# Performance work log

Measured on AMD Instinct MI355X. Metric: run time of the kernel, lower is better.

The kernel has to match this reference:

```python
import jax, jax.numpy as jnp
import numpy as np

B = 64       # graphs per batch
NPG = 1000   # nodes per graph
EPG = 8000   # edges per graph
F = 128      # num_node_features


def _lin_w(k, fi, fo):
    s = 1.0 / np.sqrt(fi)
    return jax.random.uniform(k, (fi, fo), jnp.float32, -s, s)


def setup_inputs() -> dict:
    key = jax.random.key(0)
    ks = jax.random.split(key, 40)
    N, E = B * NPG, B * EPG

    def edges(k1, k2):
        src = jax.random.randint(k1, (E,), 0, NPG)
        dst = jax.random.randint(k2, (E,), 0, NPG)
        off = (jnp.arange(E) // EPG) * NPG  # keep edges within each graph
        return jnp.stack([src + off, dst + off]).astype(jnp.int32)

    inp = {
        'x0': jax.random.normal(ks[0], (N, F), jnp.float32),
        'edge_attr0': jax.random.uniform(ks[1], (E, 4), jnp.float32),
        'edge_index0': edges(ks[2], ks[3]),
        'x1': jax.random.normal(ks[4], (N, F), jnp.float32),
        'edge_attr1': jax.random.uniform(ks[5], (E, 4), jnp.float32),
        'edge_index1': edges(ks[6], ks[7]),
        'batch0': (jnp.arange(N) // NPG).astype(jnp.int32),
        'batch1': (jnp.arange(N) // NPG).astype(jnp.int32),
        'num_graphs': B,
    }
    # GCNConv weights/biases (6 convs, all F->F)
    names = ['1A', '1B', '1C', '1D', '2', '3']
    for i, nm in enumerate(names):
        inp['W' + nm] = _lin_w(ks[8 + i], F, F)
        inp['b' + nm] = jnp.zeros((F,), jnp.float32)
    # SAGPooling score GNN (GraphConv: lin_rel with bias, lin_root no bias), 3F -> 1
    inp['Ws_rel'] = _lin_w(ks[20], 3 * F, 1)
    inp['bs_rel'] = jnp.zeros((1,), jnp.float32)
    inp['Ws_root'] = _lin_w(ks[21], 3 * F, 1)
    # MLP: 6F -> 32 -> 8 -> 2
    inp['Wm1'] = _lin_w(ks[22], 6 * F, 32)
    inp['bm1'] = jnp.zeros((32,), jnp.float32)
    inp['Wm2'] = _lin_w(ks[23], 32, 8)
    inp['bm2'] = jnp.zeros((8,), jnp.float32)
    inp['Wm3'] = _lin_w(ks[24], 8, 2)
    inp['bm3'] = jnp.zeros((2,), jnp.float32)
    return inp


def gcn_conv(x, W, b, row, col, ew):
    # PyG GCNConv: add self-loops (w=1), symmetric norm, gather->scatter-add
    N = x.shape[0]
    h = x @ W  # [N, F]
    sl = jnp.arange(N)
    row_f = jnp.concatenate([row, sl])
    col_f = jnp.concatenate([col, sl])
    w_f = jnp.concatenate([ew, jnp.ones((N,), x.dtype)])
    deg = jax.ops.segment_sum(w_f, col_f, num_segments=N)
    dinv = jnp.where(deg > 0, jax.lax.rsqrt(jnp.maximum(deg, 1e-12)), 0.0)
    norm = (dinv[row_f] * w_f * dinv[col_f])[:, None]
    return jax.ops.segment_sum(h[row_f] * norm, col_f, num_segments=N) + b


def reference(x0, edge_attr0, edge_index0, x1, edge_attr1, edge_index1,
              batch0, batch1, num_graphs,
              W1A, b1A, W1B, b1B, W1C, b1C, W1D, b1D, W2, b2, W3, b3,
              Ws_rel, bs_rel, Ws_root, Wm1, bm1, Wm2, bm2, Wm3, bm3):
    Bn = int(num_graphs)

    def branch(x, ea, ei):
        row, col = ei[0], ei[1]
        N = x.shape[0]
        ones_e = jnp.ones((ei.shape[1],), x.dtype)
        xa = jax.nn.relu(gcn_conv(x, W1A, b1A, row, col, ea[:, 0]))
        xb = jax.nn.relu(gcn_conv(x, W1B, b1B, row, col, ea[:, 1]))
        xc = jax.nn.relu(gcn_conv(x, W1C, b1C, row, col, ea[:, 2]))
        xd = jax.nn.relu(gcn_conv(x, W1D, b1D, row, col, ea[:, 3]))
        g1 = (xa + xb + xc + xd) * 0.25
        g2 = jax.nn.relu(gcn_conv(g1, W2, b2, row, col, ones_e))
        g3 = gcn_conv(g2, W3, b3, row, col, ones_e)
        g = jnp.concatenate([g1, g2, g3], axis=1)  # [N, 3F]
        # SAGPooling score via GraphConv (sum aggr, no norm/self-loops)
        agg = jax.ops.segment_sum(g[row], col, num_segments=N)
        score = (agg @ Ws_rel + bs_rel + g @ Ws_root)[:, 0]  # [N]
        npg = N // Bn
        k = npg // 2  # ratio=0.5, even graph size
        sv, si = jax.lax.top_k(score.reshape(Bn, npg), k)
        gg = g.reshape(Bn, npg, g.shape[1])
        sel = jnp.take_along_axis(gg, si[..., None], axis=1)  # [B, k, 3F]
        pooled = sel * jnp.tanh(sv)[..., None]
        return pooled.mean(axis=1)  # global_mean_pool -> [B, 3F]

    r0 = branch(x0, edge_attr0, edge_index0)
    r1 = branch(x1, edge_attr1, edge_index1)
    r = jnp.concatenate([r0, r1], axis=1)  # [B, 6F]
    h = jax.nn.relu(r @ Wm1 + bm1)
    h = jax.nn.relu(h @ Wm2 + bm2)
    return h @ Wm3 + bm3  # [B, 2]
```

## Files before the change

### kernel.cpp

```cpp
#include <hip/hip_runtime.h>
#include <math.h>


#define TPB 256

__device__ __forceinline__ int swz_block(int bid, int nb) {
  int per = nb >> 3;
  return (bid & 7) * per + (bid >> 3);
}

__device__ __forceinline__ void f4fma(float4& a, const float4 b, float s) {
  a.x += b.x * s; a.y += b.y * s; a.z += b.z * s; a.w += b.w * s;
}
__device__ __forceinline__ float4 f4s(const float4 a, float s) {
  return make_float4(a.x * s, a.y * s, a.z * s, a.w * s);
}

__global__ __launch_bounds__(TPB) void count_k(const int* __restrict__ col,
                                               int* __restrict__ cnt, int E) {
  int e = blockIdx.x * TPB + threadIdx.x;
  if (e < E) atomicAdd(&cnt[col[e]], 1);
}

__global__ __launch_bounds__(TPB) void scan1_k(const int* __restrict__ cnt,
                                               int* __restrict__ rowptr,
                                               int* __restrict__ bsum, int N) {
  __shared__ int s[TPB];
  int tid = threadIdx.x;
  int gid = blockIdx.x * TPB + tid;
  int v = (gid < N) ? cnt[gid] : 0;
  s[tid] = v;
  __syncthreads();
  for (int o = 1; o < TPB; o <<= 1) {
    int t = (tid >= o) ? s[tid - o] : 0;
    __syncthreads();
    s[tid] += t;
    __syncthreads();
  }
  if (gid < N) rowptr[gid] = s[tid] - v;
  if (tid == TPB - 1) bsum[blockIdx.x] = s[TPB - 1];
}

__global__ __launch_bounds__(TPB) void scan2_k(int* __restrict__ bsum, int nb) {
  __shared__ int s[TPB];
  int tid = threadIdx.x;
  int v = (tid < nb) ? bsum[tid] : 0;
  s[tid] = v;
  __syncthreads();
  for (int o = 1; o < TPB; o <<= 1) {
    int t = (tid >= o) ? s[tid - o] : 0;
    __syncthreads();
    s[tid] += t;
    __syncthreads();
  }
  if (tid < nb) bsum[tid] = s[tid] - v;
}

__global__ __launch_bounds__(TPB) void scan3_k(int* __restrict__ rowptr,
                                               const int* __restrict__ bsum,
                                               int N, int E) {
  int gid = blockIdx.x * TPB + threadIdx.x;
  if (gid < N) rowptr[gid] += bsum[blockIdx.x];
  if (gid == 0) rowptr[N] = E;
}

__global__ __launch_bounds__(TPB) void fill_k(const int* __restrict__ col,
                                              const int* __restrict__ rowptr,
                                              int* __restrict__ fil,
                                              int* __restrict__ csr, int E) {
  int e = blockIdx.x * TPB + threadIdx.x;
  if (e < E) {
    int c = col[e];
    int p = rowptr[c] + atomicAdd(&fil[c], 1);
    csr[p] = e;
  }
}

__global__ __launch_bounds__(TPB) void sortadj_k(const int* __restrict__ rowptr,
                                                 int* __restrict__ csr, int N) {
  int i = blockIdx.x * TPB + threadIdx.x;
  if (i >= N) return;
  int s = rowptr[i], e = rowptr[i + 1];
  for (int a = s + 1; a < e; ++a) {
    int v = csr[a];
    int b = a - 1;
    while (b >= s && csr[b] > v) { csr[b + 1] = csr[b]; --b; }
    csr[b + 1] = v;
  }
}

__global__ __launch_bounds__(TPB) void deg_k(const int* __restrict__ rowptr,
                                             const int* __restrict__ csr,
                                             const float* __restrict__ ea,
                                             float* __restrict__ dinv, int N) {
  int i = blockIdx.x * TPB + threadIdx.x;
  if (i >= N) return;
  int s = rowptr[i], e = rowptr[i + 1];
  float d0 = 1.f, d1 = 1.f, d2 = 1.f, d3 = 1.f;
  for (int j = s; j < e; ++j) {
    int eid = csr[j];
    float4 w = *reinterpret_cast<const float4*>(&ea[(size_t)eid * 4]);
    d0 += w.x; d1 += w.y; d2 += w.z; d3 += w.w;
  }
  float dO = (float)(e - s) + 1.f;
  dinv[0 * N + i] = 1.f / sqrtf(d0);
  dinv[1 * N + i] = 1.f / sqrtf(d1);
  dinv[2 * N + i] = 1.f / sqrtf(d2);
  dinv[3 * N + i] = 1.f / sqrtf(d3);
  dinv[4 * N + i] = 1.f / sqrtf(dO);
}

__global__ __launch_bounds__(TPB) void eresolve_k(
    const int* __restrict__ csr, const int* __restrict__ erow,
    const float* __restrict__ ea, const float* __restrict__ dinv, int N, int E,
    int* __restrict__ csrSrc, float4* __restrict__ csrW,
    float* __restrict__ csrWO) {
  int j = blockIdx.x * TPB + threadIdx.x;
  if (j >= E) return;
  int eid = csr[j];
  int r = erow[eid];
  float4 a = *reinterpret_cast<const float4*>(&ea[(size_t)eid * 4]);
  csrSrc[j] = r;
  csrW[j] = make_float4(a.x * dinv[r], a.y * dinv[N + r], a.z * dinv[2 * N + r],
                        a.w * dinv[3 * N + r]);
  csrWO[j] = dinv[4 * N + r];
}

__global__ __launch_bounds__(256) void gather4_k(
    const float4* __restrict__ X, const int* __restrict__ rowptr,
    const int* __restrict__ csrSrc, const float4* __restrict__ csrW,
    const float* __restrict__ dinv, int N, float4* __restrict__ S0,
    float4* __restrict__ S1, float4* __restrict__ S2, float4* __restrict__ S3) {
  int sb = swz_block(blockIdx.x, gridDim.x);
  int node = sb * 8 + (threadIdx.x >> 5);
  int l = threadIdx.x & 31;
  int s = rowptr[node], e = rowptr[node + 1];
  float d0 = dinv[node], d1 = dinv[N + node], d2 = dinv[2 * N + node],
        d3 = dinv[3 * N + node];
  float4 xs = X[(size_t)node * 32 + l];
  float4 a0 = f4s(xs, d0), a1 = f4s(xs, d1), a2 = f4s(xs, d2), a3 = f4s(xs, d3);
  int j = s;
  for (; j + 3 < e; j += 4) {
    int r0 = csrSrc[j], r1 = csrSrc[j + 1], r2 = csrSrc[j + 2], r3 = csrSrc[j + 3];
    float4 w0 = csrW[j], w1 = csrW[j + 1], w2 = csrW[j + 2], w3 = csrW[j + 3];
    float4 x0 = X[(size_t)r0 * 32 + l];
    float4 x1 = X[(size_t)r1 * 32 + l];
    float4 x2 = X[(size_t)r2 * 32 + l];
    float4 x3 = X[(size_t)r3 * 32 + l];
    f4fma(a0, x0, w0.x); f4fma(a1, x0, w0.y); f4fma(a2, x0, w0.z); f4fma(a3, x0, w0.w);
    f4fma(a0, x1, w1.x); f4fma(a1, x1, w1.y); f4fma(a2, x1, w1.z); f4fma(a3, x1, w1.w);
    f4fma(a0, x2, w2.x); f4fma(a1, x2, w2.y); f4fma(a2, x2, w2.z); f4fma(a3, x2, w2.w);
    f4fma(a0, x3, w3.x); f4fma(a1, x3, w3.y); f4fma(a2, x3, w3.z); f4fma(a3, x3, w3.w);
  }
  for (; j < e; ++j) {
    int r = csrSrc[j];
    float4 w = csrW[j];
    float4 xr = X[(size_t)r * 32 + l];
    f4fma(a0, xr, w.x); f4fma(a1, xr, w.y); f4fma(a2, xr, w.z); f4fma(a3, xr, w.w);
  }
  size_t o = (size_t)node * 32 + l;
  S0[o] = f4s(a0, d0);
  S1[o] = f4s(a1, d1);
  S2[o] = f4s(a2, d2);
  S3[o] = f4s(a3, d3);
}

__global__ __launch_bounds__(256) void gather1_k(
    const float4* __restrict__ X, const int* __restrict__ rowptr,
    const int* __restrict__ csrSrc, const float* __restrict__ csrWO,
    const float* __restrict__ dinvO, int N, float4* __restrict__ Out) {
  int sb = swz_block(blockIdx.x, gridDim.x);
  int node = sb * 8 + (threadIdx.x >> 5);
  int l = threadIdx.x & 31;
  int s = rowptr[node], e = rowptr[node + 1];
  float di = dinvO[node];
  float4 acc = f4s(X[(size_t)node * 32 + l], di);
  int j = s;
  for (; j + 3 < e; j += 4) {
    int r0 = csrSrc[j], r1 = csrSrc[j + 1], r2 = csrSrc[j + 2], r3 = csrSrc[j + 3];
    float w0 = csrWO[j], w1 = csrWO[j + 1], w2 = csrWO[j + 2], w3 = csrWO[j + 3];
    float4 x0 = X[(size_t)r0 * 32 + l];
    float4 x1 = X[(size_t)r1 * 32 + l];
    float4 x2 = X[(size_t)r2 * 32 + l];
    float4 x3 = X[(size_t)r3 * 32 + l];
    f4fma(acc, x0, w0); f4fma(acc, x1, w1); f4fma(acc, x2, w2); f4fma(acc, x3, w3);
  }
  for (; j < e; ++j) {
    f4fma(acc, X[(size_t)csrSrc[j] * 32 + l], csrWO[j]);
  }
  Out[(size_t)node * 32 + l] = f4s(acc, di);
}

template <bool RELU>
__global__ __launch_bounds__(256) void gemm_epi(const float* __restrict__ A,
                                                const float* __restrict__ W,
                                                const float* __restrict__ bias,
                                                float* __restrict__ C, int M) {
  __shared__ float As[64][64];
  __shared__ float Ws[64][128];
  int tid = threadIdx.x;
  int tx = tid & 31;
  int ty = tid >> 5;
  int rowBase = blockIdx.x * 64;
  float acc[8][4] = {};
  for (int kc = 0; kc < 128; kc += 64) {
#pragma unroll
    for (int i = 0; i < 4; ++i) {
      int idx = tid + i * 256;
      int r = idx >> 4;
      int c4 = idx & 15;
      *reinterpret_cast<float4*>(&As[r][c4 * 4]) =
          *reinterpret_cast<const float4*>(&A[(size_t)(rowBase + r) * 128 + kc + c4 * 4]);
    }
#pragma unroll
    for (int i = 0; i < 8; ++i) {
      int idx = tid + i * 256;
      int r = idx >> 5;
      int c4 = idx & 31;
      *reinterpret_cast<float4*>(&Ws[r][c4 * 4]) =
          *reinterpret_cast<const float4*>(&W[(size_t)(kc + r) * 128 + c4 * 4]);
    }
    __syncthreads();
#pragma unroll 4
    for (int k = 0; k < 64; ++k) {
      float b0[4];
      *reinterpret_cast<float4*>(b0) = *reinterpret_cast<const float4*>(&Ws[k][tx * 4]);
#pragma unroll
      for (int j = 0; j < 8; ++j) {
        float a = As[ty * 8 + j][k];
        acc[j][0] += a * b0[0];
        acc[j][1] += a * b0[1];
        acc[j][2] += a * b0[2];
        acc[j][3] += a * b0[3];
      }
    }
    __syncthreads();
  }
  float4 bq = *reinterpret_cast<const float4*>(&bias[tx * 4]);
#pragma unroll
  for (int j = 0; j < 8; ++j) {
    float v0 = acc[j][0] + bq.x, v1 = acc[j][1] + bq.y, v2 = acc[j][2] + bq.z,
          v3 = acc[j][3] + bq.w;
    if (RELU) {
      v0 = fmaxf(v0, 0.f); v1 = fmaxf(v1, 0.f); v2 = fmaxf(v2, 0.f); v3 = fmaxf(v3, 0.f);
    }
    size_t r = (size_t)(rowBase + ty * 8 + j) * 128 + tx * 4;
    *reinterpret_cast<float4*>(&C[r]) = make_float4(v0, v1, v2, v3);
  }
}

__global__ __launch_bounds__(256) void gemm4_k(
    const float* __restrict__ S0, const float* __restrict__ S1,
    const float* __restrict__ S2, const float* __restrict__ S3,
    const float* __restrict__ W0, const float* __restrict__ W1,
    const float* __restrict__ W2, const float* __restrict__ W3,
    const float* __restrict__ B0, const float* __restrict__ B1,
    const float* __restrict__ B2, const float* __restrict__ B3,
    float* __restrict__ g1, int M) {
  __shared__ float As[64][64];
  __shared__ float Ws[64][128];
  const float* Sarr[4] = {S0, S1, S2, S3};
  const float* Warr[4] = {W0, W1, W2, W3};
  const float* Barr[4] = {B0, B1, B2, B3};
  int tid = threadIdx.x;
  int tx = tid & 31;
  int ty = tid >> 5;
  int rowBase = blockIdx.x * 64;
  float facc[8][4] = {};
#pragma unroll
  for (int q = 0; q < 4; ++q) {
    const float* A = Sarr[q];
    const float* W = Warr[q];
    float acc[8][4] = {};
    for (int kc = 0; kc < 128; kc += 64) {
#pragma unroll
      for (int i = 0; i < 4; ++i) {
        int idx = tid + i * 256;
        int r = idx >> 4;
        int c4 = idx & 15;
        *reinterpret_cast<float4*>(&As[r][c4 * 4]) =
            *reinterpret_cast<const float4*>(&A[(size_t)(rowBase + r) * 128 + kc + c4 * 4]);
      }
#pragma unroll
      for (int i = 0; i < 8; ++i) {
        int idx = tid + i * 256;
        int r = idx >> 5;
        int c4 = idx & 31;
        *reinterpret_cast<float4*>(&Ws[r][c4 * 4]) =
            *reinterpret_cast<const float4*>(&W[(size_t)(kc + r) * 128 + c4 * 4]);
      }
      __syncthreads();
#pragma unroll 4
      for (int k = 0; k < 64; ++k) {
        float b0[4];
        *reinterpret_cast<float4*>(b0) = *reinterpret_cast<const float4*>(&Ws[k][tx * 4]);
#pragma unroll
        for (int j = 0; j < 8; ++j) {
          float a = As[ty * 8 + j][k];
          acc[j][0] += a * b0[0];
          acc[j][1] += a * b0[1];
          acc[j][2] += a * b0[2];
          acc[j][3] += a * b0[3];
        }
      }
      __syncthreads();
    }
    float4 bq = *reinterpret_cast<const float4*>(&Barr[q][tx * 4]);
#pragma unroll
    for (int j = 0; j < 8; ++j) {
      facc[j][0] += fmaxf(acc[j][0] + bq.x, 0.f) * 0.25f;
      facc[j][1] += fmaxf(acc[j][1] + bq.y, 0.f) * 0.25f;
      facc[j][2] += fmaxf(acc[j][2] + bq.z, 0.f) * 0.25f;
      facc[j][3] += fmaxf(acc[j][3] + bq.w, 0.f) * 0.25f;
    }
  }
#pragma unroll
  for (int j = 0; j < 8; ++j) {
    size_t r = (size_t)(rowBase + ty * 8 + j) * 128 + tx * 4;
    *reinterpret_cast<float4*>(&g1[r]) =
        make_float4(facc[j][0], facc[j][1], facc[j][2], facc[j][3]);
  }
}

__global__ __launch_bounds__(256) void score_a(
    const float* __restrict__ g1, const float* __restrict__ g2,
    const float* __restrict__ g3, const float* __restrict__ Wrel,
    const float* __restrict__ Wroot, float* __restrict__ trel,
    float* __restrict__ troot, int N) {
  int wave = threadIdx.x >> 6;
  int lane = threadIdx.x & 63;
  int node = blockIdx.x * 4 + wave;
  if (node >= N) return;
  float sr = 0.f, so = 0.f;
#pragma unroll
  for (int t = 0; t < 2; ++t) {
    int f = lane + t * 64;
    float v1 = g1[(size_t)node * 128 + f];
    float v2 = g2[(size_t)node * 128 + f];
    float v3 = g3[(size_t)node * 128 + f];
    sr += v1 * Wrel[f] + v2 * Wrel[128 + f] + v3 * Wrel[256 + f];
    so += v1 * Wroot[f] + v2 * Wroot[128 + f] + v3 * Wroot[256 + f];
  }
  for (int off = 32; off; off >>= 1) {
    sr += __shfl_down(sr, off);
    so += __shfl_down(so, off);
  }
  if (lane == 0) { trel[node] = sr; troot[node] = so; }
}

__global__ __launch_bounds__(TPB) void score_b(
    const int* __restrict__ rowptr, const int* __restrict__ csrSrc,
    const float* __restrict__ trel, const float* __restrict__ troot,
    const float* __restrict__ bs, float* __restrict__ score, int N) {
  int i = blockIdx.x * TPB + threadIdx.x;
  if (i >= N) return;
  float sc = bs[0] + troot[i];
  int s = rowptr[i], e = rowptr[i + 1];
  for (int j = s; j < e; ++j) sc += trel[csrSrc[j]];
  score[i] = sc;
}

__global__ __launch_bounds__(512) void topk_pool(
    const float* __restrict__ score, const float* __restrict__ g1,
    const float* __restrict__ g2, const float* __restrict__ g3,
    float* __restrict__ r, int half, int npg, int k) {
  __shared__ float key[1024];
  __shared__ int idx[1024];
  __shared__ float wts[512];
  int b = blockIdx.x;
  int tid = threadIdx.x;
  int base = b * npg;
  for (int i = tid; i < 1024; i += 512) {
    key[i] = (i < npg) ? score[base + i] : -3.0e38f;
    idx[i] = i;
  }
  __syncthreads();
  for (int kk = 2; kk <= 1024; kk <<= 1) {
    for (int j = kk >> 1; j > 0; j >>= 1) {
      for (int i = tid; i < 1024; i += 512) {
        int ixj = i ^ j;
        if (ixj > i) {
          bool desc = ((i & kk) == 0);
          float ki = key[i], kj = key[ixj];
          bool sw = desc ? (ki < kj) : (ki > kj);
          if (sw) {
            key[i] = kj; key[ixj] = ki;
            int t = idx[i]; idx[i] = idx[ixj]; idx[ixj] = t;
          }
        }
      }
      __syncthreads();
    }
  }
  if (tid < k) wts[tid] = tanhf(key[tid]);
  __syncthreads();
  if (tid < 384) {
    const float* gp = (tid < 128) ? g1 : ((tid < 256) ? g2 : g3);
    int fo = tid & 127;
    float acc = 0.f;
    for (int j = 0; j < k; ++j) {
      int n = base + idx[j];
      acc += wts[j] * gp[(size_t)n * 128 + fo];
    }
    r[(size_t)b * 768 + half * 384 + tid] = acc / (float)k;
  }
}

__global__ __launch_bounds__(64) void mlp_k(
    const float* __restrict__ r, const float* __restrict__ Wm1,
    const float* __restrict__ bm1, const float* __restrict__ Wm2,
    const float* __restrict__ bm2, const float* __restrict__ Wm3,
    const float* __restrict__ bm3, float* __restrict__ out) {
  __shared__ float rr[768];
  __shared__ float h1[32];
  __shared__ float h2[8];
  int b = blockIdx.x;
  int tid = threadIdx.x;
  for (int i = tid; i < 768; i += 64) rr[i] = r[(size_t)b * 768 + i];
  __syncthreads();
  if (tid < 32) {
    float s = bm1[tid];
    for (int i = 0; i < 768; ++i) s += rr[i] * Wm1[i * 32 + tid];
    h1[tid] = fmaxf(s, 0.f);
  }
  __syncthreads();
  if (tid < 8) {
    float s = bm2[tid];
    for (int i = 0; i < 32; ++i) s += h1[i] * Wm2[i * 8 + tid];
    h2[tid] = fmaxf(s, 0.f);
  }
  __syncthreads();
  if (tid < 2) {
    float s = bm3[tid];
    for (int i = 0; i < 8; ++i) s += h2[i] * Wm3[i * 2 + tid];
    out[b * 2 + tid] = s;
  }
}

extern "C" void kernel_launch(void* const* d_in, const int* in_sizes, int n_in,
                              void* d_out, int out_size, void* d_ws, size_t ws_size,
                              hipStream_t stream) {
  const float* x[2]  = {(const float*)d_in[0], (const float*)d_in[3]};
  const float* eat[2] = {(const float*)d_in[1], (const float*)d_in[4]};
  const int*   ei[2] = {(const int*)d_in[2], (const int*)d_in[5]};
  const int N = in_sizes[0] / 128;
  const int E = in_sizes[2] / 2;
  const int Bg = 64;
  const int npg = N / Bg;
  const int kq = npg / 2;

  const float* W1[4] = {(const float*)d_in[9], (const float*)d_in[11],
                        (const float*)d_in[13], (const float*)d_in[15]};
  const float* b1[4] = {(const float*)d_in[10], (const float*)d_in[12],
                        (const float*)d_in[14], (const float*)d_in[16]};
  const float* W2 = (const float*)d_in[17];
  const float* b2 = (const float*)d_in[18];
  const float* W3 = (const float*)d_in[19];
  const float* b3 = (const float*)d_in[20];
  const float* Wsrel  = (const float*)d_in[21];
  const float* bsrel  = (const float*)d_in[22];
  const float* Wsroot = (const float*)d_in[23];
  const float* Wm1 = (const float*)d_in[24];
  const float* bm1 = (const float*)d_in[25];
  const float* Wm2 = (const float*)d_in[26];
  const float* bm2 = (const float*)d_in[27];
  const float* Wm3 = (const float*)d_in[28];
  const float* bm3 = (const float*)d_in[29];
  float* out = (float*)d_out;

  char* ws = (char*)d_ws;
  size_t off = 0;
  auto alloc = [&](size_t bytes) -> void* {
    void* p = ws + off;
    off = (off + bytes + 511) & ~(size_t)511;
    return p;
  };
  const size_t nf = (size_t)N * 128 * sizeof(float);
  float* P0 = (float*)alloc(nf);
  float* P1 = (float*)alloc(nf);
  float* P2 = (float*)alloc(nf);
  float* P3 = (float*)alloc(nf);
  float* P4 = (float*)alloc(nf);
  float* dinv = (float*)alloc((size_t)5 * N * sizeof(float));
  float* trel = (float*)alloc((size_t)N * sizeof(float));
  float* trot = (float*)alloc((size_t)N * sizeof(float));
  float* sco  = (float*)alloc((size_t)N * sizeof(float));
  int* rowptr = (int*)alloc((size_t)(N + 1) * sizeof(int));
  int* cnt    = (int*)alloc((size_t)N * sizeof(int));
  int* csr    = (int*)alloc((size_t)E * sizeof(int));
  int* csrSrc = (int*)alloc((size_t)E * sizeof(int));
  float4* csrW = (float4*)alloc((size_t)E * sizeof(float4));
  float* csrWO = (float*)alloc((size_t)E * sizeof(float));
  int* bsum   = (int*)alloc(1024);
  float* rbuf = (float*)alloc((size_t)Bg * 768 * sizeof(float));
  if (off > ws_size) return;

  const int nbN = (N + TPB - 1) / TPB;
  const int nbE = (E + TPB - 1) / TPB;
  const int nbGather = N / 8;
  const int nbGemm = N / 64;

  for (int br = 0; br < 2; ++br) {
    const int* erow = ei[br];
    const int* ecol = ei[br] + E;

    hipMemsetAsync(cnt, 0, (size_t)N * sizeof(int), stream);
    count_k<<<nbE, TPB, 0, stream>>>(ecol, cnt, E);
    scan1_k<<<nbN, TPB, 0, stream>>>(cnt, rowptr, bsum, N);
    scan2_k<<<1, TPB, 0, stream>>>(bsum, nbN);
    scan3_k<<<nbN, TPB, 0, stream>>>(rowptr, bsum, N, E);
    hipMemsetAsync(cnt, 0, (size_t)N * sizeof(int), stream);
    fill_k<<<nbE, TPB, 0, stream>>>(ecol, rowptr, cnt, csr, E);
    sortadj_k<<<nbN, TPB, 0, stream>>>(rowptr, csr, N);
    deg_k<<<nbN, TPB, 0, stream>>>(rowptr, csr, eat[br], dinv, N);
    eresolve_k<<<nbE, TPB, 0, stream>>>(csr, erow, eat[br], dinv, N, E,
                                        csrSrc, csrW, csrWO);

    gather4_k<<<nbGather, 256, 0, stream>>>(
        (const float4*)x[br], rowptr, csrSrc, csrW, dinv, N,
        (float4*)P0, (float4*)P1, (float4*)P2, (float4*)P3);
    gemm4_k<<<nbGemm, 256, 0, stream>>>(P0, P1, P2, P3,
                                        W1[0], W1[1], W1[2], W1[3],
                                        b1[0], b1[1], b1[2], b1[3], P4, N);

    gather1_k<<<nbGather, 256, 0, stream>>>(
        (const float4*)P4, rowptr, csrSrc, csrWO, dinv + (size_t)4 * N, N,
        (float4*)P0);
    gemm_epi<true><<<nbGemm, 256, 0, stream>>>(P0, W2, b2, P1, N);

    gather1_k<<<nbGather, 256, 0, stream>>>(
        (const float4*)P1, rowptr, csrSrc, csrWO, dinv + (size_t)4 * N, N,
        (float4*)P0);
    gemm_epi<false><<<nbGemm, 256, 0, stream>>>(P0, W3, b3, P2, N);

    score_a<<<(N + 3) / 4, 256, 0, stream>>>(P4, P1, P2, Wsrel, Wsroot, trel, trot, N);
    score_b<<<nbN, TPB, 0, stream>>>(rowptr, csrSrc, trel, trot, bsrel, sco, N);
    topk_pool<<<Bg, 512, 0, stream>>>(sco, P4, P1, P2, rbuf, br, npg, kq);
  }

  mlp_k<<<Bg, 64, 0, stream>>>(rbuf, Wm1, bm1, Wm2, bm2, Wm3, bm3, out);
}
```

Measured before the change: 950.1 us.

## Retile dense GEMMs to 128-row tiles with 8x8 register blocking and transposed A

Both GEMM kernels move from 64-row tiles with 8x4 per-thread outputs to 128-row tiles with 8x8 per-thread outputs over a K chunk of 32. A is stored transposed in shared memory with padding, so each thread reads its A and W fragments as float4 vectors. The aim is more FMAs per shared-memory load and better register reuse. In exchange, each thread holds more registers (64 accumulators, plus 64 more in gemm4), the block count is halved, and there are more sync rounds.

```diff
diff --git a/kernel.cpp b/kernel.cpp
--- a/kernel.cpp
+++ b/kernel.cpp
@@ -191,61 +191,79 @@
   Out[(size_t)node * 32 + l] = f4s(acc, di);
 }
 
+#define GEMM_STAGE(Aptr)                                                        \
+  {                                                                             \
+    _Pragma("unroll")                                                           \
+    for (int i = 0; i < 4; ++i) {                                               \
+      int u = tid + i * 256;                                                    \
+      int r = u >> 3, k4 = u & 7;                                               \
+      float4 v = *reinterpret_cast<const float4*>(                              \
+          &Aptr[(size_t)(rowBase + r) * 128 + kc + k4 * 4]);                    \
+      AsT[k4 * 4 + 0][r] = v.x;                                                 \
+      AsT[k4 * 4 + 1][r] = v.y;                                                 \
+      AsT[k4 * 4 + 2][r] = v.z;                                                 \
+      AsT[k4 * 4 + 3][r] = v.w;                                                 \
+    }                                                                           \
+    _Pragma("unroll")                                                           \
+    for (int i = 0; i < 4; ++i) {                                               \
+      int u = tid + i * 256;                                                    \
+      int r = u >> 5, c4 = u & 31;                                              \
+      *reinterpret_cast<float4*>(&Ws[r][c4 * 4]) =                              \
+          *reinterpret_cast<const float4*>(&Wp[(size_t)(kc + r) * 128 + c4 * 4]);\
+    }                                                                           \
+  }
+
+#define GEMM_COMPUTE()                                                          \
+  _Pragma("unroll 8")                                                           \
+  for (int k = 0; k < 32; ++k) {                                                \
+    float a[8], b[8];                                                           \
+    *reinterpret_cast<float4*>(&a[0]) =                                         \
+        *reinterpret_cast<const float4*>(&AsT[k][ty * 8]);                      \
+    *reinterpret_cast<float4*>(&a[4]) =                                         \
+        *reinterpret_cast<const float4*>(&AsT[k][ty * 8 + 4]);                  \
+    *reinterpret_cast<float4*>(&b[0]) =                                         \
+        *reinterpret_cast<const float4*>(&Ws[k][tx * 8]);                       \
+    *reinterpret_cast<float4*>(&b[4]) =                                         \
+        *reinterpret_cast<const float4*>(&Ws[k][tx * 8 + 4]);                   \
+    _Pragma("unroll")                                                           \
+    for (int j = 0; j < 8; ++j) {                                               \
+      _Pragma("unroll")                                                         \
+      for (int c = 0; c < 8; ++c) acc[j][c] += a[j] * b[c];                     \
+    }                                                                           \
+  }
+
 template <bool RELU>
 __global__ __launch_bounds__(256) void gemm_epi(const float* __restrict__ A,
-                                                const float* __restrict__ W,
+                                                const float* __restrict__ Wp,
                                                 const float* __restrict__ bias,
                                                 float* __restrict__ C, int M) {
-  __shared__ float As[64][64];
-  __shared__ float Ws[64][128];
+  __shared__ float AsT[32][132];
+  __shared__ float Ws[32][128];
   int tid = threadIdx.x;
-  int tx = tid & 31;
-  int ty = tid >> 5;
-  int rowBase = blockIdx.x * 64;
-  float acc[8][4] = {};
-  for (int kc = 0; kc < 128; kc += 64) {
-#pragma unroll
-    for (int i = 0; i < 4; ++i) {
-      int idx = tid + i * 256;
-      int r = idx >> 4;
-      int c4 = idx & 15;
-      *reinterpret_cast<float4*>(&As[r][c4 * 4]) =
-          *reinterpret_cast<const float4*>(&A[(size_t)(rowBase + r) * 128 + kc + c4 * 4]);
-    }
-#pragma unroll
-    for (int i = 0; i < 8; ++i) {
-      int idx = tid + i * 256;
-      int r = idx >> 5;
-      int c4 = idx & 31;
-      *reinterpret_cast<float4*>(&Ws[r][c4 * 4]) =
-          *reinterpret_cast<const float4*>(&W[(size_t)(kc + r) * 128 + c4 * 4]);
-    }
+  int tx = tid & 15;
+  int ty = tid >> 4;
+  int rowBase = blockIdx.x * 128;
+  float acc[8][8] = {};
+  for (int kc = 0; kc < 128; kc += 32) {
+    GEMM_STAGE(A);
     __syncthreads();
-#pragma unroll 4
-    for (int k = 0; k < 64; ++k) {
-      float b0[4];
-      *reinterpret_cast<float4*>(b0) = *reinterpret_cast<const float4*>(&Ws[k][tx * 4]);
-#pragma unroll
-      for (int j = 0; j < 8; ++j) {
-        float a = As[ty * 8 + j][k];
-        acc[j][0] += a * b0[0];
-        acc[j][1] += a * b0[1];
-        acc[j][2] += a * b0[2];
-        acc[j][3] += a * b0[3];
-      }
-    }
+    GEMM_COMPUTE();
     __syncthreads();
   }
-  float4 bq = *reinterpret_cast<const float4*>(&bias[tx * 4]);
+  float bb[8];
+  *reinterpret_cast<float4*>(&bb[0]) = *reinterpret_cast<const float4*>(&bias[tx * 8]);
+  *reinterpret_cast<float4*>(&bb[4]) = *reinterpret_cast<const float4*>(&bias[tx * 8 + 4]);
 #pragma unroll
   for (int j = 0; j < 8; ++j) {
-    float v0 = acc[j][0] + bq.x, v1 = acc[j][1] + bq.y, v2 = acc[j][2] + bq.z,
-          v3 = acc[j][3] + bq.w;
-    if (RELU) {
-      v0 = fmaxf(v0, 0.f); v1 = fmaxf(v1, 0.f); v2 = fmaxf(v2, 0.f); v3 = fmaxf(v3, 0.f);
+    float o[8];
+#pragma unroll
+    for (int c = 0; c < 8; ++c) {
+      float v = acc[j][c] + bb[c];
+      o[c] = RELU ? fmaxf(v, 0.f) : v;
     }
-    size_t r = (size_t)(rowBase + ty * 8 + j) * 128 + tx * 4;
-    *reinterpret_cast<float4*>(&C[r]) = make_float4(v0, v1, v2, v3);
+    size_t r = (size_t)(rowBase + ty * 8 + j) * 128 + tx * 8;
+    *reinterpret_cast<float4*>(&C[r]) = *reinterpret_cast<float4*>(&o[0]);
+    *reinterpret_cast<float4*>(&C[r + 4]) = *reinterpret_cast<float4*>(&o[4]);
   }
 }
 
@@ -257,68 +275,42 @@
     const float* __restrict__ B0, const float* __restrict__ B1,
     const float* __restrict__ B2, const float* __restrict__ B3,
     float* __restrict__ g1, int M) {
-  __shared__ float As[64][64];
-  __shared__ float Ws[64][128];
+  __shared__ float AsT[32][132];
+  __shared__ float Ws[32][128];
   const float* Sarr[4] = {S0, S1, S2, S3};
   const float* Warr[4] = {W0, W1, W2, W3};
   const float* Barr[4] = {B0, B1, B2, B3};
   int tid = threadIdx.x;
-  int tx = tid & 31;
-  int ty = tid >> 5;
-  int rowBase = blockIdx.x * 64;
-  float facc[8][4] = {};
-#pragma unroll
+  int tx = tid & 15;
+  int ty = tid >> 4;
+  int rowBase = blockIdx.x * 128;
+  float facc[8][8] = {};
   for (int q = 0; q < 4; ++q) {
     const float* A = Sarr[q];
-    const float* W = Warr[q];
-    float acc[8][4] = {};
-    for (int kc = 0; kc < 128; kc += 64) {
-#pragma unroll
-      for (int i = 0; i < 4; ++i) {
-        int idx = tid + i * 256;
-        int r = idx >> 4;
-        int c4 = idx & 15;
-        *reinterpret_cast<float4*>(&As[r][c4 * 4]) =
-            *reinterpret_cast<const float4*>(&A[(size_t)(rowBase + r) * 128 + kc + c4 * 4]);
-      }
-#pragma unroll
-      for (int i = 0; i < 8; ++i) {
-        int idx = tid + i * 256;
-        int r = idx >> 5;
-        int c4 = idx & 31;
-        *reinterpret_cast<float4*>(&Ws[r][c4 * 4]) =
-            *reinterpret_cast<const float4*>(&W[(size_t)(kc + r) * 128 + c4 * 4]);
-      }
+    const float* Wp = Warr[q];
+    float acc[8][8] = {};
+    for (int kc = 0; kc < 128; kc += 32) {
+      GEMM_STAGE(A);
       __syncthreads();
-#pragma unroll 4
-      for (int k = 0; k < 64; ++k) {
-        float b0[4];
-        *reinterpret_cast<float4*>(b0) = *reinterpret_cast<const float4*>(&Ws[k][tx * 4]);
-#pragma unroll
-        for (int j = 0; j < 8; ++j) {
-          float a = As[ty * 8 + j][k];
-          acc[j][0] += a * b0[0];
-          acc[j][1] += a * b0[1];
-          acc[j][2] += a * b0[2];
-          acc[j][3] += a * b0[3];
-        }
-      }
+      GEMM_COMPUTE();
       __syncthreads();
     }
-    float4 bq = *reinterpret_cast<const float4*>(&Barr[q][tx * 4]);
+    float bb[8];
+    *reinterpret_cast<float4*>(&bb[0]) =
+        *reinterpret_cast<const float4*>(&Barr[q][tx * 8]);
+    *reinterpret_cast<float4*>(&bb[4]) =
+        *reinterpret_cast<const float4*>(&Barr[q][tx * 8 + 4]);
 #pragma unroll
-    for (int j = 0; j < 8; ++j) {
-      facc[j][0] += fmaxf(acc[j][0] + bq.x, 0.f) * 0.25f;
-      facc[j][1] += fmaxf(acc[j][1] + bq.y, 0.f) * 0.25f;
-      facc[j][2] += fmaxf(acc[j][2] + bq.z, 0.f) * 0.25f;
-      facc[j][3] += fmaxf(acc[j][3] + bq.w, 0.f) * 0.25f;
-    }
+    for (int j = 0; j < 8; ++j)
+#pragma unroll
+      for (int c = 0; c < 8; ++c)
+        facc[j][c] += fmaxf(acc[j][c] + bb[c], 0.f) * 0.25f;
   }
 #pragma unroll
   for (int j = 0; j < 8; ++j) {
-    size_t r = (size_t)(rowBase + ty * 8 + j) * 128 + tx * 4;
-    *reinterpret_cast<float4*>(&g1[r]) =
-        make_float4(facc[j][0], facc[j][1], facc[j][2], facc[j][3]);
+    size_t r = (size_t)(rowBase + ty * 8 + j) * 128 + tx * 8;
+    *reinterpret_cast<float4*>(&g1[r]) = *reinterpret_cast<float4*>(&facc[j][0]);
+    *reinterpret_cast<float4*>(&g1[r + 4]) = *reinterpret_cast<float4*>(&facc[j][4]);
   }
 }
 
@@ -498,7 +490,7 @@
   const int nbN = (N + TPB - 1) / TPB;
   const int nbE = (E + TPB - 1) / TPB;
   const int nbGather = N / 8;
-  const int nbGemm = N / 64;
+  const int nbGemm = N / 128;
 
   for (int br = 0; br < 2; ++br) {
     const int* erow = ei[br];
```

New measurement: 963.6 us. No clear change (+1.4%).

## Fuse neighbor gather with GEMM for the second and third GCN convs

Applied to the files above, without the earlier changes.

Merges the aggregate-then-transform pair (gather1_k then gemm_epi) into a single fconv_k kernel. Each block gathers 64 nodes' aggregated features straight into shared memory and then multiplies them by the weight matrix, so the intermediate P0 buffer is never written to or read back from global memory, and two launches per branch go away. The cost is a larger shared-memory footprint (64KB per block), which lowers occupancy, and the gather phase now runs with only 8 warps per 64 rows, which may hide latency less well than the separate gather kernel did.

```diff
diff --git a/kernel.cpp b/kernel.cpp
--- a/kernel.cpp
+++ b/kernel.cpp
@@ -165,60 +165,51 @@
   S3[o] = f4s(a3, d3);
 }
 
-__global__ __launch_bounds__(256) void gather1_k(
+template <bool RELU>
+__global__ __launch_bounds__(256) void fconv_k(
     const float4* __restrict__ X, const int* __restrict__ rowptr,
     const int* __restrict__ csrSrc, const float* __restrict__ csrWO,
-    const float* __restrict__ dinvO, int N, float4* __restrict__ Out) {
-  int sb = swz_block(blockIdx.x, gridDim.x);
-  int node = sb * 8 + (threadIdx.x >> 5);
-  int l = threadIdx.x & 31;
-  int s = rowptr[node], e = rowptr[node + 1];
-  float di = dinvO[node];
-  float4 acc = f4s(X[(size_t)node * 32 + l], di);
-  int j = s;
-  for (; j + 3 < e; j += 4) {
-    int r0 = csrSrc[j], r1 = csrSrc[j + 1], r2 = csrSrc[j + 2], r3 = csrSrc[j + 3];
-    float w0 = csrWO[j], w1 = csrWO[j + 1], w2 = csrWO[j + 2], w3 = csrWO[j + 3];
-    float4 x0 = X[(size_t)r0 * 32 + l];
-    float4 x1 = X[(size_t)r1 * 32 + l];
-    float4 x2 = X[(size_t)r2 * 32 + l];
-    float4 x3 = X[(size_t)r3 * 32 + l];
-    f4fma(acc, x0, w0); f4fma(acc, x1, w1); f4fma(acc, x2, w2); f4fma(acc, x3, w3);
-  }
-  for (; j < e; ++j) {
-    f4fma(acc, X[(size_t)csrSrc[j] * 32 + l], csrWO[j]);
-  }
-  Out[(size_t)node * 32 + l] = f4s(acc, di);
-}
-
-template <bool RELU>
-__global__ __launch_bounds__(256) void gemm_epi(const float* __restrict__ A,
-                                                const float* __restrict__ W,
-                                                const float* __restrict__ bias,
-                                                float* __restrict__ C, int M) {
-  __shared__ float As[64][64];
+    const float* __restrict__ dinvO, const float* __restrict__ Wp,
+    const float* __restrict__ bias, float* __restrict__ C, int N) {
+  __shared__ float As[64][128];
   __shared__ float Ws[64][128];
   int tid = threadIdx.x;
+  int sb = swz_block(blockIdx.x, gridDim.x);
+  int rowBase = sb * 64;
+  int l = tid & 31;
+
+  for (int g = tid >> 5; g < 64; g += 8) {
+    int node = rowBase + g;
+    int s = rowptr[node], e = rowptr[node + 1];
+    float di = dinvO[node];
+    float4 acc = f4s(X[(size_t)node * 32 + l], di);
+    int j = s;
+    for (; j + 3 < e; j += 4) {
+      int r0 = csrSrc[j], r1 = csrSrc[j + 1], r2 = csrSrc[j + 2], r3 = csrSrc[j + 3];
+      float w0 = csrWO[j], w1 = csrWO[j + 1], w2 = csrWO[j + 2], w3 = csrWO[j + 3];
+      float4 x0 = X[(size_t)r0 * 32 + l];
+      float4 x1 = X[(size_t)r1 * 32 + l];
+      float4 x2 = X[(size_t)r2 * 32 + l];
+      float4 x3 = X[(size_t)r3 * 32 + l];
+      f4fma(acc, x0, w0); f4fma(acc, x1, w1); f4fma(acc, x2, w2); f4fma(acc, x3, w3);
+    }
+    for (; j < e; ++j) {
+      f4fma(acc, X[(size_t)csrSrc[j] * 32 + l], csrWO[j]);
+    }
+    *reinterpret_cast<float4*>(&As[g][l * 4]) = f4s(acc, di);
+  }
+  __syncthreads();
+
   int tx = tid & 31;
   int ty = tid >> 5;
-  int rowBase = blockIdx.x * 64;
   float acc[8][4] = {};
   for (int kc = 0; kc < 128; kc += 64) {
 #pragma unroll
-    for (int i = 0; i < 4; ++i) {
-      int idx = tid + i * 256;
-      int r = idx >> 4;
-      int c4 = idx & 15;
-      *reinterpret_cast<float4*>(&As[r][c4 * 4]) =
-          *reinterpret_cast<const float4*>(&A[(size_t)(rowBase + r) * 128 + kc + c4 * 4]);
-    }
-#pragma unroll
     for (int i = 0; i < 8; ++i) {
-      int idx = tid + i * 256;
-      int r = idx >> 5;
-      int c4 = idx & 31;
+      int u = tid + i * 256;
+      int r = u >> 5, c4 = u & 31;
       *reinterpret_cast<float4*>(&Ws[r][c4 * 4]) =
-          *reinterpret_cast<const float4*>(&W[(size_t)(kc + r) * 128 + c4 * 4]);
+          *reinterpret_cast<const float4*>(&Wp[(size_t)(kc + r) * 128 + c4 * 4]);
     }
     __syncthreads();
 #pragma unroll 4
@@ -227,7 +218,7 @@
       *reinterpret_cast<float4*>(b0) = *reinterpret_cast<const float4*>(&Ws[k][tx * 4]);
 #pragma unroll
       for (int j = 0; j < 8; ++j) {
-        float a = As[ty * 8 + j][k];
+        float a = As[ty * 8 + j][kc + k];
         acc[j][0] += a * b0[0];
         acc[j][1] += a * b0[1];
         acc[j][2] += a * b0[2];
@@ -523,15 +514,13 @@
                                         W1[0], W1[1], W1[2], W1[3],
                                         b1[0], b1[1], b1[2], b1[3], P4, N);
 
-    gather1_k<<<nbGather, 256, 0, stream>>>(
-        (const float4*)P4, rowptr, csrSrc, csrWO, dinv + (size_t)4 * N, N,
-        (float4*)P0);
-    gemm_epi<true><<<nbGemm, 256, 0, stream>>>(P0, W2, b2, P1, N);
-
-    gather1_k<<<nbGather, 256, 0, stream>>>(
-        (const float4*)P1, rowptr, csrSrc, csrWO, dinv + (size_t)4 * N, N,
-        (float4*)P0);
-    gemm_epi<false><<<nbGemm, 256, 0, stream>>>(P0, W3, b3, P2, N);
+    fconv_k<true><<<nbGemm, 256, 0, stream>>>(
+        (const float4*)P4, rowptr, csrSrc, csrWO, dinv + (size_t)4 * N,
+        W2, b2, P1, N);
+
+    fconv_k<false><<<nbGemm, 256, 0, stream>>>(
+        (const float4*)P1, rowptr, csrSrc, csrWO, dinv + (size_t)4 * N,
+        W3, b3, P2, N);
 
     score_a<<<(N + 3) / 4, 256, 0, stream>>>(P4, P1, P2, Wsrel, Wsroot, trel, trot, N);
     score_b<<<nbN, TPB, 0, stream>>>(rowptr, csrSrc, trel, trot, bsrel, sco, N);
```

After: 975.8 us. 1.03x slower.
